# Optimization experiments

Measured on AMD Instinct MI355X. Metric: run time of the kernel, lower is better.

Reference implementation:

```python
import jax, jax.numpy as jnp
import numpy as np

H, D, C, K, N, B = 16, 64, 1024, 256, 4096, 2

def setup_inputs() -> dict:
    key = jax.random.key(0)
    ks = jax.random.split(key, 10)
    s = lambda k, shp, fan: jax.random.normal(k, shp, jnp.float32) * (1.0 / np.sqrt(fan))
    return {
        "x": jax.random.normal(ks[0], (B, N, C), jnp.float32),
        "Wq": s(ks[1], (H, D, C), C),   # per-head Linear(channels->dim), no bias
        "Wk": s(ks[2], (H, D, C), C),
        "Wv": s(ks[3], (H, D, C), C),
        "We": s(ks[4], (H, K, N), N),   # E: Linear(input_size->dim_k)
        "bE": jnp.zeros((H, K), jnp.float32),
        "Wf": s(ks[5], (H, K, N), N),   # F: Linear(input_size->dim_k)
        "bF": jnp.zeros((H, K), jnp.float32),
        "Wo": s(ks[6], (C, H * D), H * D),
        "bo": jnp.zeros((C,), jnp.float32),
    }

def reference(x, Wq, Wk, Wv, We, bE, Wf, bF, Wo, bo):
    b, n, c = x.shape
    h, d = Wq.shape[0], Wq.shape[1]
    # per-head Q/K/V projections, vectorized over heads: [b,h,n,d]
    Q = jnp.einsum('bnc,hdc->bhnd', x, Wq)
    Kt = jnp.einsum('bnc,hdc->bhdn', x, Wk)   # K already transposed(1,2)
    Vt = jnp.einsum('bnc,hdc->bhdn', x, Wv)   # V transposed(1,2)
    # Linformer E/F low-rank projections along sequence axis -> [b,h,d,k]
    Ke = jnp.einsum('bhdn,hkn->bhdk', Kt, We) + bE[None, :, None, :]
    Vf = jnp.einsum('bhdn,hkn->bhdk', Vt, Wf) + bF[None, :, None, :]
    # scaled scores + softmax over low-rank dim k
    scores = jnp.einsum('bhnd,bhdk->bhnk', Q, Kt if False else Ke) / jnp.sqrt(jnp.asarray(d, x.dtype))
    P = jax.nn.softmax(scores, axis=-1)
    # P @ V_f^T  -> [b,h,n,d]
    out = jnp.einsum('bhnk,bhkd->bhnd', P, jnp.swapaxes(Vf, -1, -2))
    # concat heads -> [b,n,h*d]
    out = jnp.transpose(out, (0, 2, 1, 3)).reshape(b, n, h * d)
    out = jax.nn.gelu(out, approximate=False)
    return out @ Wo.T + bo
```

## Files before the change

kernel.cpp:

```cpp
#include <hip/hip_runtime.h>

typedef unsigned short u16;
typedef float f32x4 __attribute__((ext_vector_type(4)));
typedef short s16x8 __attribute__((ext_vector_type(8)));
typedef unsigned short u16x4 __attribute__((ext_vector_type(4)));

__device__ __forceinline__ u16 f2bf(float f) {
  union { float f; unsigned u; } v; v.f = f;
  unsigned r = v.u + 0x7FFFu + ((v.u >> 16) & 1u);
  return (u16)(r >> 16);
}

__device__ __forceinline__ void gload_lds16(const void* g, void* l) {
  __builtin_amdgcn_global_load_lds(
      (const __attribute__((address_space(1))) void*)g,
      (__attribute__((address_space(3))) void*)l, 16, 0, 0);
}

__global__ __launch_bounds__(256) void cast_f32_bf16(
    const float* __restrict__ src, u16* __restrict__ dst, int n4) {
  int i = blockIdx.x * 256 + threadIdx.x;
  if (i >= n4) return;
  f32x4 v = ((const f32x4*)src)[i];
  u16x4 o = { f2bf(v[0]), f2bf(v[1]), f2bf(v[2]), f2bf(v[3]) };
  ((u16x4*)dst)[i] = o;
}

template <int FINAL>
__global__ __launch_bounds__(512) void gemm_pipe(
    const u16* __restrict__ A, const u16* __restrict__ B,
    void* __restrict__ Cout, const float* __restrict__ bias,
    int K, int lda, int ldb, int ldc) {
  __shared__ char smem[4 * 8192 + 4 * 16384];
  char* sA = smem;
  char* sB = smem + 32768;
  const int tid = threadIdx.x;
  const int wid = tid >> 6, lane = tid & 63;
  const int lo = lane & 15, hi = lane >> 4;
  const int wm = wid >> 2, wn = wid & 3;
  const long brow = (long)blockIdx.y * 128;
  const long bcol = (long)blockIdx.x * 256;
  const int T = K >> 5;

  f32x4 acc[4][4] = {};

  const char* Ab = (const char*)(A + (size_t)brow * lda);
  const char* Bb = (const char*)(B + (size_t)bcol * ldb);
  const size_t ldab = (size_t)lda * 2, ldbb = (size_t)ldb * 2;

  const int aoff = wid * 1024 + lane * 16;
  const int arow = aoff >> 6, acb = aoff & 63;
  const char* asrc = Ab + (size_t)arow * ldab + (acb ^ ((arow & 3) << 4));
  const int boff0 = (wid * 2) * 1024 + lane * 16;
  const int brw0 = boff0 >> 6, bcb0 = boff0 & 63;
  const char* bsrc0 = Bb + (size_t)brw0 * ldbb + (bcb0 ^ ((brw0 & 3) << 4));
  const int boff1 = (wid * 2 + 1) * 1024 + lane * 16;
  const int brw1 = boff1 >> 6, bcb1 = boff1 & 63;
  const char* bsrc1 = Bb + (size_t)brw1 * ldbb + (bcb1 ^ ((brw1 & 3) << 4));

  int ra[4], rb[4];
#pragma unroll
  for (int m = 0; m < 4; ++m)
    ra[m] = (wm * 64 + m * 16 + lo) * 64 + ((hi * 16) ^ ((lo & 3) << 4));
#pragma unroll
  for (int n = 0; n < 4; ++n)
    rb[n] = (wn * 64 + n * 16 + lo) * 64 + ((hi * 16) ^ ((lo & 3) << 4));

#define STAGE(t)                                                         \
  {                                                                      \
    int s_ = (t) & 3;                                                    \
    size_t kb_ = (size_t)(t) << 6;                                       \
    gload_lds16(asrc + kb_, sA + s_ * 8192 + wid * 1024);                \
    gload_lds16(bsrc0 + kb_, sB + s_ * 16384 + wid * 2048);              \
    gload_lds16(bsrc1 + kb_, sB + s_ * 16384 + wid * 2048 + 1024);       \
  }

  STAGE(0); STAGE(1); STAGE(2);
  asm volatile("s_waitcnt vmcnt(6)" ::: "memory");
  __builtin_amdgcn_s_barrier();
  __builtin_amdgcn_sched_barrier(0);

  for (int t = 0; t < T; ++t) {
    const char* bufA = sA + (t & 3) * 8192;
    const char* bufB = sB + (t & 3) * 16384;
    s16x8 af[4], bf[4];
#pragma unroll
    for (int m = 0; m < 4; ++m) af[m] = *(const s16x8*)(bufA + ra[m]);
#pragma unroll
    for (int n = 0; n < 4; ++n) bf[n] = *(const s16x8*)(bufB + rb[n]);
    if (t + 3 < T) STAGE(t + 3);
    __builtin_amdgcn_s_setprio(1);
#pragma unroll
    for (int m = 0; m < 4; ++m)
#pragma unroll
      for (int n = 0; n < 4; ++n)
        acc[m][n] = __builtin_amdgcn_mfma_f32_16x16x32_bf16(af[m], bf[n], acc[m][n], 0, 0, 0);
    __builtin_amdgcn_s_setprio(0);
    int rem = T - 2 - t;
    if (rem >= 2)      asm volatile("s_waitcnt vmcnt(6)" ::: "memory");
    else if (rem == 1) asm volatile("s_waitcnt vmcnt(3)" ::: "memory");
    else               asm volatile("s_waitcnt vmcnt(0)" ::: "memory");
    __builtin_amdgcn_s_barrier();
    __builtin_amdgcn_sched_barrier(0);
  }
#undef STAGE

#pragma unroll
  for (int m = 0; m < 4; ++m) {
#pragma unroll
    for (int n = 0; n < 4; ++n) {
#pragma unroll
      for (int r = 0; r < 4; ++r) {
        size_t row = brow + wm * 64 + m * 16 + hi * 4 + r;
        size_t col = bcol + wn * 64 + n * 16 + lo;
        float v = acc[m][n][r];
        if (FINAL) ((float*)Cout)[row * ldc + col] = v + bias[col];
        else       ((u16*)Cout)[row * ldc + col] = f2bf(v);
      }
    }
  }
}

__global__ __launch_bounds__(256) void kevf_kernel(
    const float* __restrict__ We, const float* __restrict__ Wf,
    const u16* __restrict__ QKV, float* __restrict__ part) {
  __shared__ u16 Wa[2][64 * 32];
  __shared__ u16 Vt[2][64 * 32];
  const int type = blockIdx.z >> 2, ns = blockIdx.z & 3;
  const int bh = blockIdx.y, b = bh >> 4, h = bh & 15;
  const int kk0 = blockIdx.x * 64;
  const float* W = (type ? Wf : We) + ((size_t)(h * 256 + kk0)) * 4096;
  const int col0 = (type ? 2048 : 1024) + h * 64;
  const int tid = threadIdx.x, wid = tid >> 6, lane = tid & 63;
  const int lo = lane & 15, hi = lane >> 4;
  const int nbeg = ns << 10;

  const int r = tid >> 2, c8 = (tid & 3) * 8;
  const int n = tid >> 3, dd0 = (tid & 7) * 8;
  const float* Wrow = W + (size_t)r * 4096 + nbeg + c8;
  const u16* Qrow = QKV + (size_t)(b * 4096 + nbeg + n) * 3072 + col0 + dd0;
  const int wslot = r * 64 + ((c8 * 2) ^ ((r & 3) << 4));
  const int rr = wid * 16 + lo;
  const int raoff = rr * 64 + ((hi * 16) ^ ((rr & 3) << 4));

  f32x4 acc[4] = {};
  f32x4 wA0, wA1, wB0, wB1;
  s16x8 qA, qB;

#define KISSUE(t, W0, W1, Q)                                        \
  { const float* wp_ = Wrow + (size_t)(t) * 32;                     \
    W0 = *(const f32x4*)wp_;                                        \
    W1 = *(const f32x4*)(wp_ + 4);                                  \
    Q = *(const s16x8*)(Qrow + (size_t)(t) * 32 * 3072); }

#define KSTAGE(bf_, W0, W1, Q)                                      \
  { s16x8 wv;                                                       \
    wv[0] = (short)f2bf(W0[0]); wv[1] = (short)f2bf(W0[1]);         \
    wv[2] = (short)f2bf(W0[2]); wv[3] = (short)f2bf(W0[3]);         \
    wv[4] = (short)f2bf(W1[0]); wv[5] = (short)f2bf(W1[1]);         \
    wv[6] = (short)f2bf(W1[2]); wv[7] = (short)f2bf(W1[3]);         \
    *(s16x8*)((char*)Wa[bf_] + wslot) = wv;                         \
    _Pragma("unroll")                                               \
    for (int q = 0; q < 8; ++q) {                                   \
      int dd = dd0 + q;                                             \
      Vt[bf_][dd * 32 + (n ^ (((dd >> 3) & 3) << 3))] = (u16)Q[q];  \
    } }

#define KCOMPUTE(bf_)                                               \
  { s16x8 a = *(const s16x8*)((const char*)Wa[bf_] + raoff);        \
    _Pragma("unroll")                                               \
    for (int dt = 0; dt < 4; ++dt) {                                \
      int dd = dt * 16 + lo;                                        \
      s16x8 bv = *(const s16x8*)&Vt[bf_][dd * 32 + ((hi * 8) ^ (((dd >> 3) & 3) << 3))]; \
      acc[dt] = __builtin_amdgcn_mfma_f32_16x16x32_bf16(a, bv, acc[dt], 0, 0, 0); \
    } }

  KISSUE(0, wA0, wA1, qA);
  KISSUE(1, wB0, wB1, qB);
#pragma unroll 1
  for (int tp = 0; tp < 15; ++tp) {
    asm volatile("s_waitcnt vmcnt(3)" ::: "memory");
    KSTAGE(0, wA0, wA1, qA);
    __syncthreads();
    KISSUE(2 * tp + 2, wA0, wA1, qA);
    KCOMPUTE(0);
    asm volatile("s_waitcnt vmcnt(3)" ::: "memory");
    KSTAGE(1, wB0, wB1, qB);
    __syncthreads();
    KISSUE(2 * tp + 3, wB0, wB1, qB);
    KCOMPUTE(1);
  }
  asm volatile("s_waitcnt vmcnt(3)" ::: "memory");
  KSTAGE(0, wA0, wA1, qA);
  __syncthreads();
  KCOMPUTE(0);
  asm volatile("s_waitcnt vmcnt(0)" ::: "memory");
  KSTAGE(1, wB0, wB1, qB);
  __syncthreads();
  KCOMPUTE(1);
#undef KISSUE
#undef KSTAGE
#undef KCOMPUTE

  const size_t pbase = ((size_t)((type * 32 + bh) * 4 + blockIdx.x) * 4 + ns) * 4096;
#pragma unroll
  for (int dt = 0; dt < 4; ++dt)
#pragma unroll
    for (int rg = 0; rg < 4; ++rg) {
      int kkl = wid * 16 + hi * 4 + rg;
      int dd = dt * 16 + lo;
      part[pbase + kkl * 64 + dd] = acc[dt][rg];
    }
}

__global__ __launch_bounds__(256) void kevf_reduce(
    const float* __restrict__ part, const float* __restrict__ bE,
    const float* __restrict__ bF, u16* __restrict__ KeT, u16* __restrict__ Vf) {
  const int tb = blockIdx.x;
  const int type = tb >> 7, bh = (tb >> 2) & 31, kc = tb & 3;
  const int t = threadIdx.x;
  const int kkl = t >> 2, dd0 = (t & 3) * 16;
  const float* p = part + (size_t)tb * 16384 + kkl * 64 + dd0;
  f32x4 s[4];
#pragma unroll
  for (int j = 0; j < 4; ++j) s[j] = ((const f32x4*)p)[j];
#pragma unroll
  for (int ns = 1; ns < 4; ++ns)
#pragma unroll
    for (int j = 0; j < 4; ++j) {
      f32x4 v = ((const f32x4*)(p + ns * 4096))[j];
      s[j][0] += v[0]; s[j][1] += v[1]; s[j][2] += v[2]; s[j][3] += v[3];
    }
  const int kk = kc * 64 + kkl;
  const float bias = (type ? bF : bE)[(bh & 15) * 256 + kk];
  if (type == 0) {
    u16* o = KeT + ((size_t)bh * 256 + kk) * 64 + dd0;
#pragma unroll
    for (int j = 0; j < 4; ++j) {
      u16x4 w = { f2bf(s[j][0] + bias), f2bf(s[j][1] + bias),
                  f2bf(s[j][2] + bias), f2bf(s[j][3] + bias) };
      *(u16x4*)(o + j * 4) = w;
    }
  } else {
#pragma unroll
    for (int j = 0; j < 4; ++j)
#pragma unroll
      for (int e = 0; e < 4; ++e) {
        int dd = dd0 + j * 4 + e;
        Vf[((size_t)bh * 64 + dd) * 256 + kk] = f2bf(s[j][e] + bias);
      }
  }
}

__global__ __launch_bounds__(256) void attn_fused(
    const u16* __restrict__ QKV, const u16* __restrict__ KeT,
    const u16* __restrict__ Vf, u16* __restrict__ attn) {
  __shared__ char smem[65536];
  char* sKe = smem;
  char* sVf = smem + 32768;
  const int tid = threadIdx.x, wid = tid >> 6, lane = tid & 63;
  const int lo = lane & 15, hi = lane >> 4;
  const int bh = blockIdx.y, b = bh >> 4, h = bh & 15;
  const int n0 = blockIdx.x * 64;

  const char* keg = (const char*)(KeT + (size_t)bh * 256 * 64);
  const char* vfg = (const char*)(Vf + (size_t)bh * 64 * 256);
#pragma unroll
  for (int i = 0; i < 8; ++i) {
    int ob = wid * 8192 + i * 1024;
    int o = ob + lane * 16;
    int kr = o >> 7, kc = o & 127;
    gload_lds16(keg + kr * 128 + (kc ^ ((kr & 7) << 4)), sKe + ob);
    int vr = o >> 9, vc = o & 511;
    gload_lds16(vfg + vr * 512 + (vc ^ ((vr & 7) << 4)), sVf + ob);
  }
  const u16* qp = QKV + (size_t)(b * 4096 + n0 + wid * 16 + lo) * 3072 + h * 64;
  s16x8 qf0 = *(const s16x8*)(qp + hi * 8);
  s16x8 qf1 = *(const s16x8*)(qp + 32 + hi * 8);
  __syncthreads();

  f32x4 sc[16];
#pragma unroll
  for (int nt = 0; nt < 16; ++nt) {
    int kk = nt * 16 + lo;
    int sw = (kk & 7) << 4;
    s16x8 b0 = *(const s16x8*)(sKe + kk * 128 + ((hi * 16) ^ sw));
    s16x8 b1 = *(const s16x8*)(sKe + kk * 128 + ((64 + hi * 16) ^ sw));
    f32x4 c = {0.f, 0.f, 0.f, 0.f};
    c = __builtin_amdgcn_mfma_f32_16x16x32_bf16(qf0, b0, c, 0, 0, 0);
    c = __builtin_amdgcn_mfma_f32_16x16x32_bf16(qf1, b1, c, 0, 0, 0);
    sc[nt] = c;
  }
  float mx[4], inv[4];
#pragma unroll
  for (int r = 0; r < 4; ++r) {
    float m = sc[0][r];
#pragma unroll
    for (int nt = 1; nt < 16; ++nt) m = fmaxf(m, sc[nt][r]);
    m = fmaxf(m, __shfl_xor(m, 1));
    m = fmaxf(m, __shfl_xor(m, 2));
    m = fmaxf(m, __shfl_xor(m, 4));
    m = fmaxf(m, __shfl_xor(m, 8));
    mx[r] = m;
  }
  const float SCL = 0.125f * 1.4426950408889634f;
  float sm[4] = {0.f, 0.f, 0.f, 0.f};
#pragma unroll
  for (int nt = 0; nt < 16; ++nt)
#pragma unroll
    for (int r = 0; r < 4; ++r) {
      float p = exp2f((sc[nt][r] - mx[r]) * SCL);
      sc[nt][r] = p;
      sm[r] += p;
    }
#pragma unroll
  for (int r = 0; r < 4; ++r) {
    float s = sm[r];
    s += __shfl_xor(s, 1);
    s += __shfl_xor(s, 2);
    s += __shfl_xor(s, 4);
    s += __shfl_xor(s, 8);
    inv[r] = 1.0f / s;
  }
  __syncthreads();
  char* pb = smem + wid * 8192;
#pragma unroll
  for (int nt = 0; nt < 16; ++nt)
#pragma unroll
    for (int r = 0; r < 4; ++r) {
      int row = hi * 4 + r;
      int kk = nt * 16 + lo;
      *(u16*)(pb + row * 512 + ((kk * 2) ^ ((row & 7) << 4))) = f2bf(sc[nt][r] * inv[r]);
    }
  __syncthreads();
  s16x8 pa[8];
#pragma unroll
  for (int ks = 0; ks < 8; ++ks)
    pa[ks] = *(const s16x8*)(pb + lo * 512 + ((ks * 64 + hi * 16) ^ ((lo & 7) << 4)));
#pragma unroll
  for (int dt = 0; dt < 4; ++dt) {
    int dd = dt * 16 + lo;
    int sw = (dd & 7) << 4;
    f32x4 o = {0.f, 0.f, 0.f, 0.f};
#pragma unroll
    for (int ks = 0; ks < 8; ++ks) {
      s16x8 vb = *(const s16x8*)(sVf + dd * 512 + ((ks * 64 + hi * 16) ^ sw));
      o = __builtin_amdgcn_mfma_f32_16x16x32_bf16(pa[ks], vb, o, 0, 0, 0);
    }
#pragma unroll
    for (int r = 0; r < 4; ++r) {
      int row = n0 + wid * 16 + hi * 4 + r;
      float x = o[r];
      float g = 0.5f * x * (1.0f + erff(x * 0.7071067811865476f));
      attn[(size_t)(b * 4096 + row) * 1024 + h * 64 + dd] = f2bf(g);
    }
  }
}

extern "C" void kernel_launch(void* const* d_in, const int* in_sizes, int n_in,
                              void* d_out, int out_size, void* d_ws, size_t ws_size,
                              hipStream_t stream) {
  const float* x  = (const float*)d_in[0];
  const float* Wq = (const float*)d_in[1];
  const float* Wk = (const float*)d_in[2];
  const float* Wv = (const float*)d_in[3];
  const float* We = (const float*)d_in[4];
  const float* bE = (const float*)d_in[5];
  const float* Wf = (const float*)d_in[6];
  const float* bF = (const float*)d_in[7];
  const float* Wo = (const float*)d_in[8];
  const float* bo = (const float*)d_in[9];
  float* out = (float*)d_out;

  char* ws = (char*)d_ws;
  u16* xb   = (u16*)(ws);
  u16* Wqkv = (u16*)(ws + 16777216);
  u16* Wob  = (u16*)(ws + 23068672);
  u16* QKV  = (u16*)(ws + 25165824);
  u16* KeT  = (u16*)(ws + 75497472);
  u16* Vf   = (u16*)(ws + 76546048);
  u16* attn = (u16*)(ws + 77594624);
  float* part = (float*)(ws);

  cast_f32_bf16<<<8192, 256, 0, stream>>>(x, xb, 2097152);
  cast_f32_bf16<<<1024, 256, 0, stream>>>(Wq, Wqkv, 262144);
  cast_f32_bf16<<<1024, 256, 0, stream>>>(Wk, Wqkv + 1048576, 262144);
  cast_f32_bf16<<<1024, 256, 0, stream>>>(Wv, Wqkv + 2097152, 262144);
  cast_f32_bf16<<<1024, 256, 0, stream>>>(Wo, Wob, 262144);

  gemm_pipe<0><<<dim3(12, 64), 512, 0, stream>>>(xb, Wqkv, QKV, nullptr,
                                                 1024, 1024, 1024, 3072);
  kevf_kernel<<<dim3(4, 32, 8), 256, 0, stream>>>(We, Wf, QKV, part);
  kevf_reduce<<<256, 256, 0, stream>>>(part, bE, bF, KeT, Vf);
  attn_fused<<<dim3(64, 32), 256, 0, stream>>>(QKV, KeT, Vf, attn);
  gemm_pipe<1><<<dim3(4, 64), 512, 0, stream>>>(attn, Wob, out, bo,
                                                1024, 1024, 1024, 1024);
}
```

Baseline: 216.4 us.

## Shrink GEMM tiles to 128x128 with 4 waves and 3-stage LDS pipeline

After: 203.9 us. -5.8%, faster.

```diff
diff --git a/kernel.cpp b/kernel.cpp
--- a/kernel.cpp
+++ b/kernel.cpp
@@ -27,19 +27,17 @@
 }
 
 template <int FINAL>
-__global__ __launch_bounds__(512) void gemm_pipe(
+__global__ __launch_bounds__(256) void gemm_pipe(
     const u16* __restrict__ A, const u16* __restrict__ B,
     void* __restrict__ Cout, const float* __restrict__ bias,
     int K, int lda, int ldb, int ldc) {
-  __shared__ char smem[4 * 8192 + 4 * 16384];
-  char* sA = smem;
-  char* sB = smem + 32768;
+  __shared__ char smem[3 * 16384];
   const int tid = threadIdx.x;
   const int wid = tid >> 6, lane = tid & 63;
   const int lo = lane & 15, hi = lane >> 4;
-  const int wm = wid >> 2, wn = wid & 3;
+  const int wr = wid >> 1, wc = wid & 1;
   const long brow = (long)blockIdx.y * 128;
-  const long bcol = (long)blockIdx.x * 256;
+  const long bcol = (long)blockIdx.x * 128;
   const int T = K >> 5;
 
   f32x4 acc[4][4] = {};
@@ -48,47 +46,50 @@
   const char* Bb = (const char*)(B + (size_t)bcol * ldb);
   const size_t ldab = (size_t)lda * 2, ldbb = (size_t)ldb * 2;
 
-  const int aoff = wid * 1024 + lane * 16;
-  const int arow = aoff >> 6, acb = aoff & 63;
-  const char* asrc = Ab + (size_t)arow * ldab + (acb ^ ((arow & 3) << 4));
-  const int boff0 = (wid * 2) * 1024 + lane * 16;
-  const int brw0 = boff0 >> 6, bcb0 = boff0 & 63;
-  const char* bsrc0 = Bb + (size_t)brw0 * ldbb + (bcb0 ^ ((brw0 & 3) << 4));
-  const int boff1 = (wid * 2 + 1) * 1024 + lane * 16;
-  const int brw1 = boff1 >> 6, bcb1 = boff1 & 63;
-  const char* bsrc1 = Bb + (size_t)brw1 * ldbb + (bcb1 ^ ((brw1 & 3) << 4));
+  const int La0 = wid * 2048 + lane * 16;
+  const int La1 = La0 + 1024;
+  const int ar0 = La0 >> 6, ac0 = (La0 & 63) ^ (((La0 >> 7) & 3) << 4);
+  const int ar1 = La1 >> 6, ac1 = (La1 & 63) ^ (((La1 >> 7) & 3) << 4);
+  const char* asrc0 = Ab + (size_t)ar0 * ldab + ac0;
+  const char* asrc1 = Ab + (size_t)ar1 * ldab + ac1;
+  const char* bsrc0 = Bb + (size_t)ar0 * ldbb + ac0;
+  const char* bsrc1 = Bb + (size_t)ar1 * ldbb + ac1;
 
   int ra[4], rb[4];
 #pragma unroll
-  for (int m = 0; m < 4; ++m)
-    ra[m] = (wm * 64 + m * 16 + lo) * 64 + ((hi * 16) ^ ((lo & 3) << 4));
-#pragma unroll
-  for (int n = 0; n < 4; ++n)
-    rb[n] = (wn * 64 + n * 16 + lo) * 64 + ((hi * 16) ^ ((lo & 3) << 4));
-
-#define STAGE(t)                                                         \
-  {                                                                      \
-    int s_ = (t) & 3;                                                    \
-    size_t kb_ = (size_t)(t) << 6;                                       \
-    gload_lds16(asrc + kb_, sA + s_ * 8192 + wid * 1024);                \
-    gload_lds16(bsrc0 + kb_, sB + s_ * 16384 + wid * 2048);              \
-    gload_lds16(bsrc1 + kb_, sB + s_ * 16384 + wid * 2048 + 1024);       \
-  }
-
-  STAGE(0); STAGE(1); STAGE(2);
-  asm volatile("s_waitcnt vmcnt(6)" ::: "memory");
+  for (int m = 0; m < 4; ++m) {
+    int row = wr * 64 + m * 16 + lo;
+    ra[m] = row * 64 + ((hi ^ ((row >> 1) & 3)) << 4);
+  }
+#pragma unroll
+  for (int n = 0; n < 4; ++n) {
+    int row = wc * 64 + n * 16 + lo;
+    rb[n] = 8192 + row * 64 + ((hi ^ ((row >> 1) & 3)) << 4);
+  }
+
+#define STAGE(t)                                                    \
+  {                                                                 \
+    char* ls_ = smem + ((t) % 3) * 16384;                           \
+    size_t kb_ = (size_t)(t) << 6;                                  \
+    gload_lds16(asrc0 + kb_, ls_ + La0);                            \
+    gload_lds16(asrc1 + kb_, ls_ + La1);                            \
+    gload_lds16(bsrc0 + kb_, ls_ + 8192 + La0);                     \
+    gload_lds16(bsrc1 + kb_, ls_ + 8192 + La1);                     \
+  }
+
+  STAGE(0); STAGE(1);
+  asm volatile("s_waitcnt vmcnt(4)" ::: "memory");
   __builtin_amdgcn_s_barrier();
   __builtin_amdgcn_sched_barrier(0);
 
   for (int t = 0; t < T; ++t) {
-    const char* bufA = sA + (t & 3) * 8192;
-    const char* bufB = sB + (t & 3) * 16384;
+    const char* buf = smem + (t % 3) * 16384;
     s16x8 af[4], bf[4];
 #pragma unroll
-    for (int m = 0; m < 4; ++m) af[m] = *(const s16x8*)(bufA + ra[m]);
-#pragma unroll
-    for (int n = 0; n < 4; ++n) bf[n] = *(const s16x8*)(bufB + rb[n]);
-    if (t + 3 < T) STAGE(t + 3);
+    for (int m = 0; m < 4; ++m) af[m] = *(const s16x8*)(buf + ra[m]);
+#pragma unroll
+    for (int n = 0; n < 4; ++n) bf[n] = *(const s16x8*)(buf + rb[n]);
+    if (t + 2 < T) STAGE(t + 2);
     __builtin_amdgcn_s_setprio(1);
 #pragma unroll
     for (int m = 0; m < 4; ++m)
@@ -96,10 +97,8 @@
       for (int n = 0; n < 4; ++n)
         acc[m][n] = __builtin_amdgcn_mfma_f32_16x16x32_bf16(af[m], bf[n], acc[m][n], 0, 0, 0);
     __builtin_amdgcn_s_setprio(0);
-    int rem = T - 2 - t;
-    if (rem >= 2)      asm volatile("s_waitcnt vmcnt(6)" ::: "memory");
-    else if (rem == 1) asm volatile("s_waitcnt vmcnt(3)" ::: "memory");
-    else               asm volatile("s_waitcnt vmcnt(0)" ::: "memory");
+    if (t + 2 < T) asm volatile("s_waitcnt vmcnt(4)" ::: "memory");
+    else           asm volatile("s_waitcnt vmcnt(0)" ::: "memory");
     __builtin_amdgcn_s_barrier();
     __builtin_amdgcn_sched_barrier(0);
   }
@@ -111,8 +110,8 @@
     for (int n = 0; n < 4; ++n) {
 #pragma unroll
       for (int r = 0; r < 4; ++r) {
-        size_t row = brow + wm * 64 + m * 16 + hi * 4 + r;
-        size_t col = bcol + wn * 64 + n * 16 + lo;
+        size_t row = brow + wr * 64 + m * 16 + hi * 4 + r;
+        size_t col = bcol + wc * 64 + n * 16 + lo;
         float v = acc[m][n][r];
         if (FINAL) ((float*)Cout)[row * ldc + col] = v + bias[col];
         else       ((u16*)Cout)[row * ldc + col] = f2bf(v);
@@ -388,11 +387,11 @@
   cast_f32_bf16<<<1024, 256, 0, stream>>>(Wv, Wqkv + 2097152, 262144);
   cast_f32_bf16<<<1024, 256, 0, stream>>>(Wo, Wob, 262144);
 
-  gemm_pipe<0><<<dim3(12, 64), 512, 0, stream>>>(xb, Wqkv, QKV, nullptr,
+  gemm_pipe<0><<<dim3(24, 64), 256, 0, stream>>>(xb, Wqkv, QKV, nullptr,
                                                  1024, 1024, 1024, 3072);
   kevf_kernel<<<dim3(4, 32, 8), 256, 0, stream>>>(We, Wf, QKV, part);
   kevf_reduce<<<256, 256, 0, stream>>>(part, bE, bF, KeT, Vf);
   attn_fused<<<dim3(64, 32), 256, 0, stream>>>(QKV, KeT, Vf, attn);
-  gemm_pipe<1><<<dim3(4, 64), 512, 0, stream>>>(attn, Wob, out, bo,
+  gemm_pipe<1><<<dim3(8, 64), 256, 0, stream>>>(attn, Wob, out, bo,
                                                 1024, 1024, 1024, 1024);
 }
```
